# Kernel optimization log

Measured on AMD Instinct MI355X. Metric: run time of the kernel, lower is better.

Reference implementation:

```python
import jax, jax.numpy as jnp
import numpy as np

B, S, T, E, D = 16, 2048, 1024, 256, 256  # batch, src_len, tgt_len, enc_size, dec_size


def setup_inputs() -> dict:
    key = jax.random.key(0)
    k1, k2, k3, k4, k5 = jax.random.split(key, 5)
    enc_states = jax.random.normal(k1, (B, S, E), dtype=jnp.float32)
    dec_states = jax.random.normal(k2, (B, T, D), dtype=jnp.float32)
    # valid-prefix mask: each row has at least one valid (True) source position
    lengths = jax.random.randint(k3, (B,), 1, S + 1)
    src_mask = jnp.arange(S)[None, :] < lengths[:, None]  # (B, S) bool
    # Dense layer weights (no bias). Glorot-ish scale.
    W_enc = jax.random.normal(k4, (E, D), dtype=jnp.float32) / np.sqrt(E)
    W_fin = jax.random.normal(k5, (E + D, D), dtype=jnp.float32) / np.sqrt(E + D)
    return {"enc_states": enc_states, "dec_states": dec_states,
            "src_mask": src_mask, "W_enc": W_enc, "W_fin": W_fin}


def reference(enc_states, dec_states, src_mask, W_enc, W_fin):
    # enc_trnsfrmr: (B,S,E) @ (E,D) -> (B,S,D)
    enc_proj = jnp.einsum('bse,ed->bsd', enc_states, W_enc)
    # attention scores: batch_dot(dec_states, enc_proj^T) -> (B,T,S)
    scores = jnp.einsum('btd,bsd->bts', dec_states, enc_proj)
    scores = jnp.where(src_mask[:, None, :], scores, -jnp.inf)
    wts = jax.nn.softmax(scores, axis=-1)  # (B,T,S)
    # broadcast-multiply + reduce_sum == weighted sum over src positions
    context = jnp.einsum('bts,bse->bte', wts, enc_states)  # (B,T,E)
    cat = jnp.concatenate([context, dec_states], axis=-1)  # (B,T,E+D)
    return jnp.tanh(jnp.einsum('btf,fd->btd', cat, W_fin))  # (B,T,D)
```

## Files before the change

kernel.cpp:

```cpp
#include <hip/hip_runtime.h>
#include <math.h>
#include <stdint.h>

#define NB 16
#define NS 2048
#define NT 1024
#define NE 256
#define ND 256
#define NM (NB * NT)
#define KF (NE + ND)

typedef short sh8 __attribute__((ext_vector_type(8)));
typedef float f4v __attribute__((ext_vector_type(4)));

static __device__ __forceinline__ float bf2f(unsigned short u) {
    union { unsigned int i; float f; } v;
    v.i = ((unsigned int)u) << 16;
    return v.f;
}
static __device__ __forceinline__ unsigned short f2bf(float f) {
    union { unsigned int i; float f; } v;
    v.f = f;
    unsigned int x = v.i;
    x += 0x7FFFu + ((x >> 16) & 1u);
    return (unsigned short)(x >> 16);
}
static __device__ __forceinline__ float4 load4(const void* p, int isbf, long idx) {
    if (isbf) {
        const unsigned short* h = (const unsigned short*)p + idx;
        ushort4 u = *(const ushort4*)h;
        return make_float4(bf2f(u.x), bf2f(u.y), bf2f(u.z), bf2f(u.w));
    }
    const float* f = (const float*)p + idx;
    return *(const float4*)f;
}
static __device__ __forceinline__ int mvalid(const void* m, int kind, int b, int s) {
    long idx = (long)b * NS + s;
    switch (kind) {
        case 0:  return ((const unsigned char*)m)[idx] != 0;
        case 1:  return ((const int*)m)[idx] != 0;
        case 2:  return ((const unsigned short*)m)[idx] != 0;
        default: return ((const unsigned int*)m)[idx] != 0;
    }
}

__global__ void k_detect(const void* __restrict__ enc_raw,
                         const void* __restrict__ mask_raw,
                         int* __restrict__ flags) {
    __shared__ int cnt;
    if (threadIdx.x == 0) cnt = 0;
    __syncthreads();
    const unsigned short* h = (const unsigned short*)enc_raw;
    int local = 0;
    for (int i = threadIdx.x; i < 4096; i += 256) {
        int ex = (h[i] >> 7) & 0xFF;
        if (ex >= 97 && ex <= 157) local++;
    }
    atomicAdd(&cnt, local);
    __syncthreads();
    if (threadIdx.x == 0) {
        int isbf = (cnt >= 3700) ? 1 : 0;
        const unsigned char* mb = (const unsigned char*)mask_raw;
        int kind;
        if (mb[1] == 0x3F)                       kind = 2;
        else if (mb[3] == 0x3F && mb[1] == 0)    kind = 3;
        else if (mb[1] == 1)                     kind = 0;
        else if (mb[4] == 1 || mb[8] == 1)       kind = 1;
        else                                     kind = (mb[NS] == 1) ? 0 : 1;
        flags[0] = isbf;
        flags[1] = kind;
    }
}

__global__ __launch_bounds__(256) void k_split(const void* __restrict__ src,
                                               const int* __restrict__ flags,
                                               unsigned short* __restrict__ hh,
                                               unsigned short* __restrict__ ll) {
    const int isbf = flags[0];
    const long i = ((long)blockIdx.x * 256 + threadIdx.x) * 8;
    if (isbf) {
        sh8 v = *(const sh8*)((const unsigned short*)src + i);
        *(sh8*)(hh + i) = v;
    } else {
        const float* f = (const float*)src + i;
        sh8 hv, lv;
#pragma unroll
        for (int j = 0; j < 8; ++j) {
            float x = f[j];
            unsigned short h = f2bf(x);
            hv[j] = (short)h;
            lv[j] = (short)f2bf(x - bf2f(h));
        }
        *(sh8*)(hh + i) = hv;
        *(sh8*)(ll + i) = lv;
    }
}

__global__ __launch_bounds__(256) void k_twf(const void* __restrict__ Wfin,
                                             const int* __restrict__ flags,
                                             unsigned short* __restrict__ wfh,
                                             unsigned short* __restrict__ wfl) {
    const int isbf = flags[0];
    __shared__ float T[64][68];
    const int f0 = blockIdx.x * 64, n0 = blockIdx.y * 64;
    const int tid = threadIdx.x;
#pragma unroll
    for (int i = 0; i < 4; ++i) {
        int idx = tid + i * 256;
        int r = idx >> 4, c4 = (idx & 15) << 2;
        float4 v = load4(Wfin, isbf, (long)(f0 + r) * ND + n0 + c4);
        T[r][c4] = v.x; T[r][c4 + 1] = v.y; T[r][c4 + 2] = v.z; T[r][c4 + 3] = v.w;
    }
    __syncthreads();
#pragma unroll
    for (int i = 0; i < 4; ++i) {
        int idx = tid + i * 256;
        int n = idx >> 4, f4 = (idx & 15) << 2;
        ushort4 hv, lv;
        float x;
        x = T[f4 + 0][n]; hv.x = f2bf(x); lv.x = f2bf(x - bf2f(hv.x));
        x = T[f4 + 1][n]; hv.y = f2bf(x); lv.y = f2bf(x - bf2f(hv.y));
        x = T[f4 + 2][n]; hv.z = f2bf(x); lv.z = f2bf(x - bf2f(hv.z));
        x = T[f4 + 3][n]; hv.w = f2bf(x); lv.w = f2bf(x - bf2f(hv.w));
        long base = (long)(n0 + n) * KF + f0 + f4;
        *(ushort4*)&wfh[base] = hv;
        *(ushort4*)&wfl[base] = lv;
    }
}

__global__ __launch_bounds__(256) void k_q_m(const unsigned short* __restrict__ dh,
                                             const unsigned short* __restrict__ dl,
                                             const unsigned short* __restrict__ wh,
                                             const unsigned short* __restrict__ wl,
                                             const int* __restrict__ flags,
                                             unsigned short* __restrict__ qh,
                                             unsigned short* __restrict__ ql) {
    const int isbf = flags[0];
    const int tid = threadIdx.x;
    const int lane = tid & 63, wid = tid >> 6;
    const int lr = lane & 15, lg = lane >> 4;
    const int bid = blockIdx.x;
    const int mblk = (bid & 7) + (((bid >> 3) >> 2) << 3);
    const int nblk = (bid >> 3) & 3;
    const long m0 = (long)mblk * 128 + wid * 32;
    const int  n0 = nblk * 64;
    __shared__ __align__(16) unsigned short Bh_s[64][264];
    __shared__ __align__(16) unsigned short Bl_s[64][264];
    {
        const int row = tid >> 2, seg = (tid & 3) * 64;
        const unsigned short* src = wh + (long)(n0 + row) * ND + seg;
#pragma unroll
        for (int c = 0; c < 8; ++c)
            *(sh8*)&Bh_s[row][seg + c * 8] = *(const sh8*)(src + c * 8);
        if (!isbf) {
            const unsigned short* src2 = wl + (long)(n0 + row) * ND + seg;
#pragma unroll
            for (int c = 0; c < 8; ++c)
                *(sh8*)&Bl_s[row][seg + c * 8] = *(const sh8*)(src2 + c * 8);
        }
    }
    __syncthreads();
    const unsigned short* Ah = dh + (m0 + lr) * ND + lg * 8;
    const unsigned short* Al = dl + (m0 + lr) * ND + lg * 8;
    f4v acc[2][4];
#pragma unroll
    for (int i = 0; i < 2; ++i)
#pragma unroll
        for (int j = 0; j < 4; ++j) acc[i][j] = (f4v){0.f, 0.f, 0.f, 0.f};
    if (isbf) {
#pragma unroll
        for (int k8 = 0; k8 < 8; ++k8) {
            const int ko = k8 * 32;
            sh8 a0 = *(const sh8*)(Ah + ko);
            sh8 a1 = *(const sh8*)(Ah + 16 * ND + ko);
#pragma unroll
            for (int ni = 0; ni < 4; ++ni) {
                sh8 b = *(const sh8*)&Bh_s[ni * 16 + lr][ko + lg * 8];
                acc[0][ni] = __builtin_amdgcn_mfma_f32_16x16x32_bf16(a0, b, acc[0][ni], 0, 0, 0);
                acc[1][ni] = __builtin_amdgcn_mfma_f32_16x16x32_bf16(a1, b, acc[1][ni], 0, 0, 0);
            }
        }
    } else {
#pragma unroll
        for (int k8 = 0; k8 < 8; ++k8) {
            const int ko = k8 * 32;
            sh8 a0 = *(const sh8*)(Ah + ko);
            sh8 a1 = *(const sh8*)(Ah + 16 * ND + ko);
            sh8 la0 = *(const sh8*)(Al + ko);
            sh8 la1 = *(const sh8*)(Al + 16 * ND + ko);
#pragma unroll
            for (int ni = 0; ni < 4; ++ni) {
                sh8 b  = *(const sh8*)&Bh_s[ni * 16 + lr][ko + lg * 8];
                sh8 lb = *(const sh8*)&Bl_s[ni * 16 + lr][ko + lg * 8];
                acc[0][ni] = __builtin_amdgcn_mfma_f32_16x16x32_bf16(a0, b, acc[0][ni], 0, 0, 0);
                acc[0][ni] = __builtin_amdgcn_mfma_f32_16x16x32_bf16(la0, b, acc[0][ni], 0, 0, 0);
                acc[0][ni] = __builtin_amdgcn_mfma_f32_16x16x32_bf16(a0, lb, acc[0][ni], 0, 0, 0);
                acc[1][ni] = __builtin_amdgcn_mfma_f32_16x16x32_bf16(a1, b, acc[1][ni], 0, 0, 0);
                acc[1][ni] = __builtin_amdgcn_mfma_f32_16x16x32_bf16(la1, b, acc[1][ni], 0, 0, 0);
                acc[1][ni] = __builtin_amdgcn_mfma_f32_16x16x32_bf16(a1, lb, acc[1][ni], 0, 0, 0);
            }
        }
    }
#pragma unroll
    for (int mi = 0; mi < 2; ++mi)
#pragma unroll
        for (int r = 0; r < 4; ++r) {
            long rowb = (m0 + mi * 16 + lg * 4 + r) * NE + n0 + lr;
#pragma unroll
            for (int ni = 0; ni < 4; ++ni) {
                float v = acc[mi][ni][r];
                unsigned short h = f2bf(v);
                qh[rowb + ni * 16] = h;
                ql[rowb + ni * 16] = f2bf(v - bf2f(h));
            }
        }
}

__global__ __launch_bounds__(256, 2) void k_attn(
    const unsigned short* qh, const unsigned short* ql,
    const unsigned short* __restrict__ eh, const unsigned short* __restrict__ el,
    const void* __restrict__ mask, const int* __restrict__ flags,
    unsigned short* ch, unsigned short* cl,
    float* __restrict__ pctx, float* __restrict__ Mp, float* __restrict__ Lp)
{
    const int isbf  = flags[0];
    const int mkind = flags[1];
    const int b  = blockIdx.y;
    const int t0 = blockIdx.x * 32;
    const int part = blockIdx.z, nparts = gridDim.z;
    const int tid  = threadIdx.x;
    const int lane = tid & 63;
    const int wid  = tid >> 6;
    const int th = wid & 1;
    const int sh = wid >> 1;
    const int lr = lane & 15;
    const int lg = lane >> 4;

    __shared__ __align__(16) unsigned short EHR[32][264];
    __shared__ __align__(16) unsigned short ELR[32][264];
    __shared__ __align__(16) unsigned short VT[256][40];
    __shared__ __align__(16) float PBs[32][36];
    __shared__ float hm[2][32];
    __shared__ float hs[2][32];
    __shared__ int s_len;

    if (tid == 0) s_len = 0;
    __syncthreads();
    {
        int c = 0;
#pragma unroll
        for (int j = 0; j < 8; ++j) c += mvalid(mask, mkind, b, tid * 8 + j);
        atomicAdd(&s_len, c);
    }
    __syncthreads();
    const int len  = s_len;
    const int s_lo = part * (NS / nparts);
    const int s_hi = min(s_lo + NS / nparts, len);
    const int ntiles = (s_hi > s_lo) ? ((s_hi - s_lo + 31) >> 5) : 0;
    const long mrow = (long)part * NM + (long)b * NT + t0;
    if (ntiles == 0) {
        if (nparts > 1 && tid < 32) { Mp[mrow + tid] = -INFINITY; Lp[mrow + tid] = 0.f; }
        return;
    }

    sh8 qhf[8], qlf[8];
    {
        const unsigned short* qp  = qh + ((long)b * NT + t0 + th * 16 + lr) * NE + lg * 8;
        const unsigned short* qp2 = ql + ((long)b * NT + t0 + th * 16 + lr) * NE + lg * 8;
#pragma unroll
        for (int k8 = 0; k8 < 8; ++k8) {
            qhf[k8] = *(const sh8*)(qp  + k8 * 32);
            qlf[k8] = *(const sh8*)(qp2 + k8 * 32);
        }
    }

    f4v O[8];
#pragma unroll
    for (int et = 0; et < 8; ++et) O[et] = (f4v){0.f, 0.f, 0.f, 0.f};
    float Mreg4[4], L4[4], MregP = -INFINITY;
#pragma unroll
    for (int r = 0; r < 4; ++r) { Mreg4[r] = -INFINITY; L4[r] = 0.f; }

    const int ss = tid >> 3;
    const int ee = (tid & 7) * 8;

    sh8 rh[4], rl[4];
    {
        const unsigned short* eg = eh + ((long)b * NS + s_lo + ss) * NE;
#pragma unroll
        for (int c = 0; c < 4; ++c) rh[c] = *(const sh8*)(eg + ee + c * 64);
        if (!isbf) {
            const unsigned short* eg2 = el + ((long)b * NS + s_lo + ss) * NE;
#pragma unroll
            for (int c = 0; c < 4; ++c) rl[c] = *(const sh8*)(eg2 + ee + c * 64);
        }
#pragma unroll
        for (int c = 0; c < 4; ++c) {
            const int e0 = ee + c * 64;
            *(sh8*)&EHR[ss][e0] = rh[c];
            if (!isbf) *(sh8*)&ELR[ss][e0] = rl[c];
        }
    }

    for (int it = 0; it < ntiles; ++it) {
        const int s0 = s_lo + it * 32;
        __syncthreads();
        f4v cacc;
        {
            const unsigned short* ep = &EHR[sh * 16 + lr][lg * 8];
            const unsigned short* lp = &ELR[sh * 16 + lr][lg * 8];
            f4v c0 = (f4v){0.f, 0.f, 0.f, 0.f};
            f4v c1 = (f4v){0.f, 0.f, 0.f, 0.f};
            f4v c2 = (f4v){0.f, 0.f, 0.f, 0.f};
            if (isbf) {
#pragma unroll
                for (int k8 = 0; k8 < 8; ++k8) {
                    sh8 ea = *(const sh8*)(ep + k8 * 32);
                    c0 = __builtin_amdgcn_mfma_f32_16x16x32_bf16(ea, qhf[k8], c0, 0, 0, 0);
                    c1 = __builtin_amdgcn_mfma_f32_16x16x32_bf16(ea, qlf[k8], c1, 0, 0, 0);
                }
            } else {
#pragma unroll
                for (int k8 = 0; k8 < 8; ++k8) {
                    sh8 ea = *(const sh8*)(ep + k8 * 32);
                    sh8 eb = *(const sh8*)(lp + k8 * 32);
                    c0 = __builtin_amdgcn_mfma_f32_16x16x32_bf16(ea, qhf[k8], c0, 0, 0, 0);
                    c1 = __builtin_amdgcn_mfma_f32_16x16x32_bf16(ea, qlf[k8], c1, 0, 0, 0);
                    c2 = __builtin_amdgcn_mfma_f32_16x16x32_bf16(eb, qhf[k8], c2, 0, 0, 0);
                }
            }
            cacc = c0 + c1 + c2;
        }
        {
            unsigned short col[32];
#pragma unroll
            for (int s = 0; s < 32; ++s) col[s] = EHR[s][tid];
#pragma unroll
            for (int c = 0; c < 4; ++c)
                *(sh8*)&VT[tid][c * 8] = *(const sh8*)&col[c * 8];
        }
        float sc[4];
#pragma unroll
        for (int r = 0; r < 4; ++r) {
            int sl = sh * 16 + lg * 4 + r;
            sc[r] = (s0 + sl < len) ? cacc[r] : -INFINITY;
        }
        float m4 = fmaxf(fmaxf(sc[0], sc[1]), fmaxf(sc[2], sc[3]));
        m4 = fmaxf(m4, __shfl_xor(m4, 16));
        m4 = fmaxf(m4, __shfl_xor(m4, 32));
        float p[4], ps = 0.f;
#pragma unroll
        for (int r = 0; r < 4; ++r) {
            p[r] = (sc[r] == -INFINITY) ? 0.f : __expf(sc[r] - m4);
            ps += p[r];
        }
        ps += __shfl_xor(ps, 16);
        ps += __shfl_xor(ps, 32);
        if (lane < 16) { hm[sh][th * 16 + lane] = m4; hs[sh][th * 16 + lane] = ps; }
        *(float4*)&PBs[th * 16 + lr][sh * 16 + lg * 4] = make_float4(p[0], p[1], p[2], p[3]);
        const int more = (it + 1 < ntiles);
        if (more) {
            const unsigned short* eg = eh + ((long)b * NS + s0 + 32 + ss) * NE;
#pragma unroll
            for (int c = 0; c < 4; ++c) rh[c] = *(const sh8*)(eg + ee + c * 64);
            if (!isbf) {
                const unsigned short* eg2 = el + ((long)b * NS + s0 + 32 + ss) * NE;
#pragma unroll
                for (int c = 0; c < 4; ++c) rl[c] = *(const sh8*)(eg2 + ee + c * 64);
            }
        }
        __syncthreads();
        float f0, f1, al[4];
        {
            const int tP = th * 16 + lr;
            float h0 = hm[0][tP], h1 = hm[1][tP];
            float Mn = fmaxf(MregP, fmaxf(h0, h1));
            f0 = __expf(h0 - Mn);
            f1 = __expf(h1 - Mn);
            MregP = Mn;
        }
#pragma unroll
        for (int r = 0; r < 4; ++r) {
            const int t4 = th * 16 + lg * 4 + r;
            float g0 = hm[0][t4], g1 = hm[1][t4];
            float Mn = fmaxf(Mreg4[r], fmaxf(g0, g1));
            al[r] = __expf(Mreg4[r] - Mn);
            L4[r] = L4[r] * al[r] + hs[0][t4] * __expf(g0 - Mn) + hs[1][t4] * __expf(g1 - Mn);
            Mreg4[r] = Mn;
        }
        {
            const float fsc = (lg < 2) ? f0 : f1;
            f4v pA = *(const f4v*)&PBs[th * 16 + lr][lg * 8];
            f4v pB = *(const f4v*)&PBs[th * 16 + lr][lg * 8 + 4];
            sh8 pf;
#pragma unroll
            for (int j = 0; j < 4; ++j) {
                pf[j]     = (short)f2bf(pA[j] * fsc);
                pf[4 + j] = (short)f2bf(pB[j] * fsc);
            }
            f4v alv = (f4v){al[0], al[1], al[2], al[3]};
#pragma unroll
            for (int et = 0; et < 8; ++et) O[et] *= alv;
#pragma unroll
            for (int et = 0; et < 8; ++et) {
                sh8 vf = *(const sh8*)&VT[sh * 128 + et * 16 + lr][lg * 8];
                O[et] = __builtin_amdgcn_mfma_f32_16x16x32_bf16(pf, vf, O[et], 0, 0, 0);
            }
        }
        if (more) {
#pragma unroll
            for (int c = 0; c < 4; ++c) {
                const int e0 = ee + c * 64;
                *(sh8*)&EHR[ss][e0] = rh[c];
                if (!isbf) *(sh8*)&ELR[ss][e0] = rl[c];
            }
        }
    }
    if (nparts == 1) {
        f4v inv;
#pragma unroll
        for (int r = 0; r < 4; ++r) inv[r] = 1.0f / L4[r];
#pragma unroll
        for (int et = 0; et < 8; ++et) {
            f4v ov = O[et] * inv;
            long rbase = ((long)b * NT + t0 + th * 16 + lg * 4) * NE + sh * 128 + et * 16 + lr;
#pragma unroll
            for (int r = 0; r < 4; ++r) {
                float v = ov[r];
                unsigned short h = f2bf(v);
                ch[rbase + (long)r * NE] = h;
                cl[rbase + (long)r * NE] = f2bf(v - bf2f(h));
            }
        }
    } else {
        float* op = pctx + (long)part * NM * NE;
#pragma unroll
        for (int et = 0; et < 8; ++et) {
            long rbase = ((long)b * NT + t0 + th * 16 + lg * 4) * NE + sh * 128 + et * 16 + lr;
#pragma unroll
            for (int r = 0; r < 4; ++r)
                op[rbase + (long)r * NE] = O[et][r];
        }
        if (sh == 0 && lr == 0) {
#pragma unroll
            for (int r = 0; r < 4; ++r) {
                Mp[mrow + th * 16 + lg * 4 + r] = Mreg4[r];
                Lp[mrow + th * 16 + lg * 4 + r] = L4[r];
            }
        }
    }
}

__global__ __launch_bounds__(256) void k_comb(const float* __restrict__ pctx,
                                              const float* __restrict__ Mp,
                                              const float* __restrict__ Lp,
                                              int nparts,
                                              unsigned short* __restrict__ ch,
                                              unsigned short* __restrict__ cl) {
    const long m = (long)blockIdx.x * 8 + (threadIdx.x >> 5);
    const int  e0 = (threadIdx.x & 31) * 8;
    float Mv[4], Lv[4];
    float M = -INFINITY;
    for (int p = 0; p < nparts; ++p) {
        Mv[p] = Mp[(long)p * NM + m];
        Lv[p] = Lp[(long)p * NM + m];
        if (Lv[p] > 0.f) M = fmaxf(M, Mv[p]);
    }
    float L = 0.f, w[4];
    for (int p = 0; p < nparts; ++p) {
        w[p] = (Lv[p] > 0.f) ? __expf(Mv[p] - M) : 0.f;
        L += Lv[p] * w[p];
    }
    float o[8] = {};
    for (int p = 0; p < nparts; ++p) {
        if (w[p] > 0.f) {
            const float* src = pctx + (long)p * NM * NE + m * NE + e0;
            f4v a = *(const f4v*)src;
            f4v c = *(const f4v*)(src + 4);
#pragma unroll
            for (int j = 0; j < 4; ++j) { o[j] += a[j] * w[p]; o[4 + j] += c[j] * w[p]; }
        }
    }
    const float inv = 1.0f / L;
    unsigned short hv[8], lv[8];
#pragma unroll
    for (int j = 0; j < 8; ++j) {
        float v = o[j] * inv;
        unsigned short h = f2bf(v);
        hv[j] = h;
        lv[j] = f2bf(v - bf2f(h));
    }
    long base = m * NE + e0;
    *(ushort4*)&ch[base]     = *(ushort4*)&hv[0];
    *(ushort4*)&ch[base + 4] = *(ushort4*)&hv[4];
    *(ushort4*)&cl[base]     = *(ushort4*)&lv[0];
    *(ushort4*)&cl[base + 4] = *(ushort4*)&lv[4];
}

__global__ __launch_bounds__(256) void k_fin_m(const unsigned short* __restrict__ ch,
                                               const unsigned short* __restrict__ cl,
                                               const unsigned short* __restrict__ dh,
                                               const unsigned short* __restrict__ dl,
                                               const unsigned short* __restrict__ wh,
                                               const unsigned short* __restrict__ wl,
                                               const int* __restrict__ flags,
                                               void* __restrict__ out) {
    const int isbf = flags[0];
    const int tid = threadIdx.x;
    const int lane = tid & 63, wid = tid >> 6;
    const int lr = lane & 15, lg = lane >> 4;
    const int bid = blockIdx.x;
    const int mblk = (bid & 7) + (((bid >> 3) >> 2) << 3);
    const int nblk = (bid >> 3) & 3;
    const long m0 = (long)mblk * 128 + wid * 32;
    const int  n0 = nblk * 64;
    __shared__ __align__(16) unsigned short Bh_s[64][264];
    __shared__ __align__(16) unsigned short Bl_s[64][264];
    const int row = tid >> 2, seg = (tid & 3) * 64;
    f4v acc[2][4];
#pragma unroll
    for (int i = 0; i < 2; ++i)
#pragma unroll
        for (int j = 0; j < 4; ++j) acc[i][j] = (f4v){0.f, 0.f, 0.f, 0.f};

#pragma unroll
    for (int ph = 0; ph < 2; ++ph) {
        if (ph) __syncthreads();
        {
            const unsigned short* src = wh + (long)(n0 + row) * KF + ph * 256 + seg;
#pragma unroll
            for (int c = 0; c < 8; ++c)
                *(sh8*)&Bh_s[row][seg + c * 8] = *(const sh8*)(src + c * 8);
            if (!isbf) {
                const unsigned short* src2 = wl + (long)(n0 + row) * KF + ph * 256 + seg;
#pragma unroll
                for (int c = 0; c < 8; ++c)
                    *(sh8*)&Bl_s[row][seg + c * 8] = *(const sh8*)(src2 + c * 8);
            }
        }
        __syncthreads();
        const unsigned short* Ah = (ph == 0 ? ch : dh) + (m0 + lr) * 256 + lg * 8;
        const unsigned short* Al = (ph == 0 ? cl : dl) + (m0 + lr) * 256 + lg * 8;
        if (isbf) {
#pragma unroll
            for (int k8 = 0; k8 < 8; ++k8) {
                const int ko = k8 * 32;
                sh8 a0 = *(const sh8*)(Ah + ko);
                sh8 a1 = *(const sh8*)(Ah + 16 * 256 + ko);
#pragma unroll
                for (int ni = 0; ni < 4; ++ni) {
                    sh8 b = *(const sh8*)&Bh_s[ni * 16 + lr][ko + lg * 8];
                    acc[0][ni] = __builtin_amdgcn_mfma_f32_16x16x32_bf16(a0, b, acc[0][ni], 0, 0, 0);
                    acc[1][ni] = __builtin_amdgcn_mfma_f32_16x16x32_bf16(a1, b, acc[1][ni], 0, 0, 0);
                }
            }
        } else {
#pragma unroll
            for (int k8 = 0; k8 < 8; ++k8) {
                const int ko = k8 * 32;
                sh8 a0 = *(const sh8*)(Ah + ko);
                sh8 a1 = *(const sh8*)(Ah + 16 * 256 + ko);
                sh8 la0 = *(const sh8*)(Al + ko);
                sh8 la1 = *(const sh8*)(Al + 16 * 256 + ko);
#pragma unroll
                for (int ni = 0; ni < 4; ++ni) {
                    sh8 b  = *(const sh8*)&Bh_s[ni * 16 + lr][ko + lg * 8];
                    sh8 lb = *(const sh8*)&Bl_s[ni * 16 + lr][ko + lg * 8];
                    acc[0][ni] = __builtin_amdgcn_mfma_f32_16x16x32_bf16(a0, b, acc[0][ni], 0, 0, 0);
                    acc[0][ni] = __builtin_amdgcn_mfma_f32_16x16x32_bf16(la0, b, acc[0][ni], 0, 0, 0);
                    acc[0][ni] = __builtin_amdgcn_mfma_f32_16x16x32_bf16(a0, lb, acc[0][ni], 0, 0, 0);
                    acc[1][ni] = __builtin_amdgcn_mfma_f32_16x16x32_bf16(a1, b, acc[1][ni], 0, 0, 0);
                    acc[1][ni] = __builtin_amdgcn_mfma_f32_16x16x32_bf16(la1, b, acc[1][ni], 0, 0, 0);
                    acc[1][ni] = __builtin_amdgcn_mfma_f32_16x16x32_bf16(a1, lb, acc[1][ni], 0, 0, 0);
                }
            }
        }
    }
    if (isbf) {
        unsigned short* o = (unsigned short*)out;
#pragma unroll
        for (int mi = 0; mi < 2; ++mi)
#pragma unroll
            for (int r = 0; r < 4; ++r) {
                long rowb = (m0 + mi * 16 + lg * 4 + r) * ND + n0 + lr;
#pragma unroll
                for (int ni = 0; ni < 4; ++ni)
                    o[rowb + ni * 16] = f2bf(tanhf(acc[mi][ni][r]));
            }
    } else {
        float* o = (float*)out;
#pragma unroll
        for (int mi = 0; mi < 2; ++mi)
#pragma unroll
            for (int r = 0; r < 4; ++r) {
                long rowb = (m0 + mi * 16 + lg * 4 + r) * ND + n0 + lr;
#pragma unroll
                for (int ni = 0; ni < 4; ++ni)
                    o[rowb + ni * 16] = tanhf(acc[mi][ni][r]);
            }
    }
}

extern "C" void kernel_launch(void* const* d_in, const int* in_sizes, int n_in,
                              void* d_out, int out_size, void* d_ws, size_t ws_size,
                              hipStream_t stream) {
    const void* enc  = d_in[0];
    const void* dec  = d_in[1];
    const void* mask = d_in[2];
    const void* Wenc = d_in[3];
    const void* Wfin = d_in[4];

    unsigned short* ehb = (unsigned short*)d_ws;
    unsigned short* elb = ehb + (size_t)NB * NS * NE;
    unsigned short* qhb = elb + (size_t)NB * NS * NE;
    unsigned short* qlb = qhb + (size_t)NM * NE;
    unsigned short* dhb = qlb + (size_t)NM * NE;
    unsigned short* dlb = dhb + (size_t)NM * ND;
    unsigned short* weh = dlb + (size_t)NM * ND;
    unsigned short* wel = weh + (size_t)NE * ND;
    unsigned short* wfh = wel + (size_t)NE * ND;
    unsigned short* wfl = wfh + (size_t)KF * ND;
    unsigned short* wend = wfl + (size_t)KF * ND;

    const size_t fixed = (size_t)((char*)wend - (char*)d_ws);
    int parts = 1;
    for (int p = 4; p >= 1; p >>= 1) {
        size_t need = fixed + ((p > 1) ? ((size_t)p * NM * NE * 4 + (size_t)p * NM * 8) : 0) + 256;
        if (ws_size >= need) { parts = p; break; }
    }
    float* pctx = (float*)wend;
    float* Mpb  = pctx + ((parts > 1) ? (size_t)parts * NM * NE : 0);
    float* Lpb  = Mpb + (size_t)parts * NM;
    int*   flags = (int*)(Lpb + (size_t)parts * NM);

    k_detect<<<1, 256, 0, stream>>>(enc, mask, flags);
    k_split<<<(NB * NS * NE) / 2048, 256, 0, stream>>>(enc, flags, ehb, elb);
    k_split<<<(NM * ND) / 2048, 256, 0, stream>>>(dec, flags, dhb, dlb);
    k_split<<<(NE * ND) / 2048, 256, 0, stream>>>(Wenc, flags, weh, wel);
    k_twf<<<dim3(KF / 64, ND / 64), 256, 0, stream>>>(Wfin, flags, wfh, wfl);
    k_q_m<<<512, 256, 0, stream>>>(dhb, dlb, weh, wel, flags, qhb, qlb);
    k_attn<<<dim3(NT / 32, NB, parts), 256, 0, stream>>>(qhb, qlb, ehb, elb, mask, flags,
                                                         qhb, qlb, pctx, Mpb, Lpb);
    if (parts > 1)
        k_comb<<<NM / 8, 256, 0, stream>>>(pctx, Mpb, Lpb, parts, qhb, qlb);
    k_fin_m<<<512, 256, 0, stream>>>(qhb, qlb, dhb, dlb, wfh, wfl, flags, d_out);
}
```

Baseline: 266.7 us.

## Fuse fp32 split into GEMMs, precompute mask lengths, interleave attention tiles

The hi/lo bf16 split of dec_states and W_enc now happens inside the q-projection and final GEMM kernels, so two split launches and their workspace round-trips go away. The projection weights are staged through shared memory in 128-wide halves, which shrinks shared memory use. Mask lengths are computed once in the detect kernel rather than in every attention block. Source tiles are assigned to attention partitions round-robin, which balances work across partitions when rows have short valid prefixes. In exchange, fp32 conversion work is repeated across the N-blocks of each GEMM and there are more barrier phases.

```diff
diff --git a/kernel.cpp b/kernel.cpp
--- a/kernel.cpp
+++ b/kernel.cpp
@@ -43,22 +43,35 @@
         default: return ((const unsigned int*)m)[idx] != 0;
     }
 }
+static __device__ __forceinline__ void f8_to_hl(const float* p, sh8& h8, sh8& l8) {
+    f4v x0 = *(const f4v*)p;
+    f4v x1 = *(const f4v*)(p + 4);
+#pragma unroll
+    for (int j = 0; j < 4; ++j) {
+        unsigned short h = f2bf(x0[j]); h8[j] = (short)h; l8[j] = (short)f2bf(x0[j] - bf2f(h));
+        h = f2bf(x1[j]); h8[4 + j] = (short)h; l8[4 + j] = (short)f2bf(x1[j] - bf2f(h));
+    }
+}
 
 __global__ void k_detect(const void* __restrict__ enc_raw,
                          const void* __restrict__ mask_raw,
                          int* __restrict__ flags) {
     __shared__ int cnt;
-    if (threadIdx.x == 0) cnt = 0;
+    __shared__ int kindS;
+    __shared__ int lensS[16];
+    const int tid = threadIdx.x;
+    if (tid == 0) cnt = 0;
+    if (tid < 16) lensS[tid] = 0;
     __syncthreads();
     const unsigned short* h = (const unsigned short*)enc_raw;
     int local = 0;
-    for (int i = threadIdx.x; i < 4096; i += 256) {
+    for (int i = tid; i < 4096; i += 256) {
         int ex = (h[i] >> 7) & 0xFF;
         if (ex >= 97 && ex <= 157) local++;
     }
     atomicAdd(&cnt, local);
     __syncthreads();
-    if (threadIdx.x == 0) {
+    if (tid == 0) {
         int isbf = (cnt >= 3700) ? 1 : 0;
         const unsigned char* mb = (const unsigned char*)mask_raw;
         int kind;
@@ -69,7 +82,16 @@
         else                                     kind = (mb[NS] == 1) ? 0 : 1;
         flags[0] = isbf;
         flags[1] = kind;
-    }
+        kindS = kind;
+    }
+    __syncthreads();
+    const int kind = kindS;
+    const int bb = tid >> 4, sl = tid & 15;
+    int c = 0;
+    for (int j = 0; j < 128; ++j) c += mvalid(mask_raw, kind, bb, sl + j * 16);
+    atomicAdd(&lensS[bb], c);
+    __syncthreads();
+    if (tid < 16) flags[2 + tid] = lensS[tid];
 }
 
 __global__ __launch_bounds__(256) void k_split(const void* __restrict__ src,
@@ -84,13 +106,7 @@
     } else {
         const float* f = (const float*)src + i;
         sh8 hv, lv;
-#pragma unroll
-        for (int j = 0; j < 8; ++j) {
-            float x = f[j];
-            unsigned short h = f2bf(x);
-            hv[j] = (short)h;
-            lv[j] = (short)f2bf(x - bf2f(h));
-        }
+        f8_to_hl(f, hv, lv);
         *(sh8*)(hh + i) = hv;
         *(sh8*)(ll + i) = lv;
     }
@@ -128,10 +144,8 @@
     }
 }
 
-__global__ __launch_bounds__(256) void k_q_m(const unsigned short* __restrict__ dh,
-                                             const unsigned short* __restrict__ dl,
-                                             const unsigned short* __restrict__ wh,
-                                             const unsigned short* __restrict__ wl,
+__global__ __launch_bounds__(256) void k_q_m(const void* __restrict__ dec,
+                                             const void* __restrict__ Wenc,
                                              const int* __restrict__ flags,
                                              unsigned short* __restrict__ qh,
                                              unsigned short* __restrict__ ql) {
@@ -144,60 +158,67 @@
     const int nblk = (bid >> 3) & 3;
     const long m0 = (long)mblk * 128 + wid * 32;
     const int  n0 = nblk * 64;
-    __shared__ __align__(16) unsigned short Bh_s[64][264];
-    __shared__ __align__(16) unsigned short Bl_s[64][264];
-    {
-        const int row = tid >> 2, seg = (tid & 3) * 64;
-        const unsigned short* src = wh + (long)(n0 + row) * ND + seg;
-#pragma unroll
-        for (int c = 0; c < 8; ++c)
-            *(sh8*)&Bh_s[row][seg + c * 8] = *(const sh8*)(src + c * 8);
-        if (!isbf) {
-            const unsigned short* src2 = wl + (long)(n0 + row) * ND + seg;
-#pragma unroll
-            for (int c = 0; c < 8; ++c)
-                *(sh8*)&Bl_s[row][seg + c * 8] = *(const sh8*)(src2 + c * 8);
-        }
-    }
-    __syncthreads();
-    const unsigned short* Ah = dh + (m0 + lr) * ND + lg * 8;
-    const unsigned short* Al = dl + (m0 + lr) * ND + lg * 8;
+    __shared__ __align__(16) unsigned short Bh_s[64][136];
+    __shared__ __align__(16) unsigned short Bl_s[64][136];
+    const int row = tid >> 2, seg = (tid & 3) * 32;
     f4v acc[2][4];
 #pragma unroll
     for (int i = 0; i < 2; ++i)
 #pragma unroll
         for (int j = 0; j < 4; ++j) acc[i][j] = (f4v){0.f, 0.f, 0.f, 0.f};
-    if (isbf) {
-#pragma unroll
-        for (int k8 = 0; k8 < 8; ++k8) {
-            const int ko = k8 * 32;
-            sh8 a0 = *(const sh8*)(Ah + ko);
-            sh8 a1 = *(const sh8*)(Ah + 16 * ND + ko);
-#pragma unroll
-            for (int ni = 0; ni < 4; ++ni) {
-                sh8 b = *(const sh8*)&Bh_s[ni * 16 + lr][ko + lg * 8];
-                acc[0][ni] = __builtin_amdgcn_mfma_f32_16x16x32_bf16(a0, b, acc[0][ni], 0, 0, 0);
-                acc[1][ni] = __builtin_amdgcn_mfma_f32_16x16x32_bf16(a1, b, acc[1][ni], 0, 0, 0);
-            }
-        }
-    } else {
-#pragma unroll
-        for (int k8 = 0; k8 < 8; ++k8) {
-            const int ko = k8 * 32;
-            sh8 a0 = *(const sh8*)(Ah + ko);
-            sh8 a1 = *(const sh8*)(Ah + 16 * ND + ko);
-            sh8 la0 = *(const sh8*)(Al + ko);
-            sh8 la1 = *(const sh8*)(Al + 16 * ND + ko);
-#pragma unroll
-            for (int ni = 0; ni < 4; ++ni) {
-                sh8 b  = *(const sh8*)&Bh_s[ni * 16 + lr][ko + lg * 8];
-                sh8 lb = *(const sh8*)&Bl_s[ni * 16 + lr][ko + lg * 8];
-                acc[0][ni] = __builtin_amdgcn_mfma_f32_16x16x32_bf16(a0, b, acc[0][ni], 0, 0, 0);
-                acc[0][ni] = __builtin_amdgcn_mfma_f32_16x16x32_bf16(la0, b, acc[0][ni], 0, 0, 0);
-                acc[0][ni] = __builtin_amdgcn_mfma_f32_16x16x32_bf16(a0, lb, acc[0][ni], 0, 0, 0);
-                acc[1][ni] = __builtin_amdgcn_mfma_f32_16x16x32_bf16(a1, b, acc[1][ni], 0, 0, 0);
-                acc[1][ni] = __builtin_amdgcn_mfma_f32_16x16x32_bf16(la1, b, acc[1][ni], 0, 0, 0);
-                acc[1][ni] = __builtin_amdgcn_mfma_f32_16x16x32_bf16(a1, lb, acc[1][ni], 0, 0, 0);
+
+#pragma unroll
+    for (int ph = 0; ph < 2; ++ph) {
+        if (ph) __syncthreads();
+        if (isbf) {
+            const unsigned short* src = (const unsigned short*)Wenc + (long)(n0 + row) * ND + ph * 128 + seg;
+#pragma unroll
+            for (int c = 0; c < 4; ++c)
+                *(sh8*)&Bh_s[row][seg + c * 8] = *(const sh8*)(src + c * 8);
+        } else {
+            const float* src = (const float*)Wenc + (long)(n0 + row) * ND + ph * 128 + seg;
+#pragma unroll
+            for (int c = 0; c < 4; ++c) {
+                sh8 hv, lv;
+                f8_to_hl(src + c * 8, hv, lv);
+                *(sh8*)&Bh_s[row][seg + c * 8] = hv;
+                *(sh8*)&Bl_s[row][seg + c * 8] = lv;
+            }
+        }
+        __syncthreads();
+        if (isbf) {
+            const unsigned short* Ab = (const unsigned short*)dec + (m0 + lr) * ND + ph * 128 + lg * 8;
+#pragma unroll
+            for (int k8 = 0; k8 < 4; ++k8) {
+                const int ko = k8 * 32;
+                sh8 a0 = *(const sh8*)(Ab + ko);
+                sh8 a1 = *(const sh8*)(Ab + 16 * ND + ko);
+#pragma unroll
+                for (int ni = 0; ni < 4; ++ni) {
+                    sh8 b = *(const sh8*)&Bh_s[ni * 16 + lr][ko + lg * 8];
+                    acc[0][ni] = __builtin_amdgcn_mfma_f32_16x16x32_bf16(a0, b, acc[0][ni], 0, 0, 0);
+                    acc[1][ni] = __builtin_amdgcn_mfma_f32_16x16x32_bf16(a1, b, acc[1][ni], 0, 0, 0);
+                }
+            }
+        } else {
+            const float* Af = (const float*)dec + (m0 + lr) * ND + ph * 128 + lg * 8;
+#pragma unroll
+            for (int k8 = 0; k8 < 4; ++k8) {
+                const int ko = k8 * 32;
+                sh8 a0, la0, a1, la1;
+                f8_to_hl(Af + ko, a0, la0);
+                f8_to_hl(Af + 16 * ND + ko, a1, la1);
+#pragma unroll
+                for (int ni = 0; ni < 4; ++ni) {
+                    sh8 b  = *(const sh8*)&Bh_s[ni * 16 + lr][ko + lg * 8];
+                    sh8 lb = *(const sh8*)&Bl_s[ni * 16 + lr][ko + lg * 8];
+                    acc[0][ni] = __builtin_amdgcn_mfma_f32_16x16x32_bf16(a0, b, acc[0][ni], 0, 0, 0);
+                    acc[0][ni] = __builtin_amdgcn_mfma_f32_16x16x32_bf16(la0, b, acc[0][ni], 0, 0, 0);
+                    acc[0][ni] = __builtin_amdgcn_mfma_f32_16x16x32_bf16(a0, lb, acc[0][ni], 0, 0, 0);
+                    acc[1][ni] = __builtin_amdgcn_mfma_f32_16x16x32_bf16(a1, b, acc[1][ni], 0, 0, 0);
+                    acc[1][ni] = __builtin_amdgcn_mfma_f32_16x16x32_bf16(la1, b, acc[1][ni], 0, 0, 0);
+                    acc[1][ni] = __builtin_amdgcn_mfma_f32_16x16x32_bf16(a1, lb, acc[1][ni], 0, 0, 0);
+                }
             }
         }
     }
@@ -219,12 +240,11 @@
 __global__ __launch_bounds__(256, 2) void k_attn(
     const unsigned short* qh, const unsigned short* ql,
     const unsigned short* __restrict__ eh, const unsigned short* __restrict__ el,
-    const void* __restrict__ mask, const int* __restrict__ flags,
+    const int* __restrict__ flags,
     unsigned short* ch, unsigned short* cl,
     float* __restrict__ pctx, float* __restrict__ Mp, float* __restrict__ Lp)
 {
     const int isbf  = flags[0];
-    const int mkind = flags[1];
     const int b  = blockIdx.y;
     const int t0 = blockIdx.x * 32;
     const int part = blockIdx.z, nparts = gridDim.z;
@@ -242,21 +262,10 @@
     __shared__ __align__(16) float PBs[32][36];
     __shared__ float hm[2][32];
     __shared__ float hs[2][32];
-    __shared__ int s_len;
-
-    if (tid == 0) s_len = 0;
-    __syncthreads();
-    {
-        int c = 0;
-#pragma unroll
-        for (int j = 0; j < 8; ++j) c += mvalid(mask, mkind, b, tid * 8 + j);
-        atomicAdd(&s_len, c);
-    }
-    __syncthreads();
-    const int len  = s_len;
-    const int s_lo = part * (NS / nparts);
-    const int s_hi = min(s_lo + NS / nparts, len);
-    const int ntiles = (s_hi > s_lo) ? ((s_hi - s_lo + 31) >> 5) : 0;
+
+    const int len = flags[2 + b];
+    const int nT = (len + 31) >> 5;
+    const int ntiles = (nT > part) ? ((nT - part + nparts - 1) / nparts) : 0;
     const long mrow = (long)part * NM + (long)b * NT + t0;
     if (ntiles == 0) {
         if (nparts > 1 && tid < 32) { Mp[mrow + tid] = -INFINITY; Lp[mrow + tid] = 0.f; }
@@ -286,11 +295,11 @@
 
     sh8 rh[4], rl[4];
     {
-        const unsigned short* eg = eh + ((long)b * NS + s_lo + ss) * NE;
+        const unsigned short* eg = eh + ((long)b * NS + part * 32 + ss) * NE;
 #pragma unroll
         for (int c = 0; c < 4; ++c) rh[c] = *(const sh8*)(eg + ee + c * 64);
         if (!isbf) {
-            const unsigned short* eg2 = el + ((long)b * NS + s_lo + ss) * NE;
+            const unsigned short* eg2 = el + ((long)b * NS + part * 32 + ss) * NE;
 #pragma unroll
             for (int c = 0; c < 4; ++c) rl[c] = *(const sh8*)(eg2 + ee + c * 64);
         }
@@ -303,7 +312,7 @@
     }
 
     for (int it = 0; it < ntiles; ++it) {
-        const int s0 = s_lo + it * 32;
+        const int s0 = (part + it * nparts) << 5;
         __syncthreads();
         f4v cacc;
         {
@@ -360,11 +369,12 @@
         *(float4*)&PBs[th * 16 + lr][sh * 16 + lg * 4] = make_float4(p[0], p[1], p[2], p[3]);
         const int more = (it + 1 < ntiles);
         if (more) {
-            const unsigned short* eg = eh + ((long)b * NS + s0 + 32 + ss) * NE;
+            const int s0n = s0 + (nparts << 5);
+            const unsigned short* eg = eh + ((long)b * NS + s0n + ss) * NE;
 #pragma unroll
             for (int c = 0; c < 4; ++c) rh[c] = *(const sh8*)(eg + ee + c * 64);
             if (!isbf) {
-                const unsigned short* eg2 = el + ((long)b * NS + s0 + 32 + ss) * NE;
+                const unsigned short* eg2 = el + ((long)b * NS + s0n + ss) * NE;
 #pragma unroll
                 for (int c = 0; c < 4; ++c) rl[c] = *(const sh8*)(eg2 + ee + c * 64);
             }
@@ -499,8 +509,7 @@
 
 __global__ __launch_bounds__(256) void k_fin_m(const unsigned short* __restrict__ ch,
                                                const unsigned short* __restrict__ cl,
-                                               const unsigned short* __restrict__ dh,
-                                               const unsigned short* __restrict__ dl,
+                                               const void* __restrict__ dec,
                                                const unsigned short* __restrict__ wh,
                                                const unsigned short* __restrict__ wl,
                                                const int* __restrict__ flags,
@@ -514,9 +523,9 @@
     const int nblk = (bid >> 3) & 3;
     const long m0 = (long)mblk * 128 + wid * 32;
     const int  n0 = nblk * 64;
-    __shared__ __align__(16) unsigned short Bh_s[64][264];
-    __shared__ __align__(16) unsigned short Bl_s[64][264];
-    const int row = tid >> 2, seg = (tid & 3) * 64;
+    __shared__ __align__(16) unsigned short Bh_s[64][136];
+    __shared__ __align__(16) unsigned short Bl_s[64][136];
+    const int row = tid >> 2, seg = (tid & 3) * 32;
     f4v acc[2][4];
 #pragma unroll
     for (int i = 0; i < 2; ++i)
@@ -524,54 +533,86 @@
         for (int j = 0; j < 4; ++j) acc[i][j] = (f4v){0.f, 0.f, 0.f, 0.f};
 
 #pragma unroll
-    for (int ph = 0; ph < 2; ++ph) {
+    for (int ph = 0; ph < 4; ++ph) {
         if (ph) __syncthreads();
         {
-            const unsigned short* src = wh + (long)(n0 + row) * KF + ph * 256 + seg;
-#pragma unroll
-            for (int c = 0; c < 8; ++c)
+            const unsigned short* src = wh + (long)(n0 + row) * KF + ph * 128 + seg;
+#pragma unroll
+            for (int c = 0; c < 4; ++c)
                 *(sh8*)&Bh_s[row][seg + c * 8] = *(const sh8*)(src + c * 8);
             if (!isbf) {
-                const unsigned short* src2 = wl + (long)(n0 + row) * KF + ph * 256 + seg;
-#pragma unroll
-                for (int c = 0; c < 8; ++c)
+                const unsigned short* src2 = wl + (long)(n0 + row) * KF + ph * 128 + seg;
+#pragma unroll
+                for (int c = 0; c < 4; ++c)
                     *(sh8*)&Bl_s[row][seg + c * 8] = *(const sh8*)(src2 + c * 8);
             }
         }
         __syncthreads();
-        const unsigned short* Ah = (ph == 0 ? ch : dh) + (m0 + lr) * 256 + lg * 8;
-        const unsigned short* Al = (ph == 0 ? cl : dl) + (m0 + lr) * 256 + lg * 8;
-        if (isbf) {
-#pragma unroll
-            for (int k8 = 0; k8 < 8; ++k8) {
+        if (ph < 2) {
+            const unsigned short* Ah = ch + (m0 + lr) * NE + ph * 128 + lg * 8;
+            const unsigned short* Al = cl + (m0 + lr) * NE + ph * 128 + lg * 8;
+#pragma unroll
+            for (int k8 = 0; k8 < 4; ++k8) {
                 const int ko = k8 * 32;
                 sh8 a0 = *(const sh8*)(Ah + ko);
-                sh8 a1 = *(const sh8*)(Ah + 16 * 256 + ko);
-#pragma unroll
-                for (int ni = 0; ni < 4; ++ni) {
-                    sh8 b = *(const sh8*)&Bh_s[ni * 16 + lr][ko + lg * 8];
-                    acc[0][ni] = __builtin_amdgcn_mfma_f32_16x16x32_bf16(a0, b, acc[0][ni], 0, 0, 0);
-                    acc[1][ni] = __builtin_amdgcn_mfma_f32_16x16x32_bf16(a1, b, acc[1][ni], 0, 0, 0);
+                sh8 a1 = *(const sh8*)(Ah + 16 * NE + ko);
+                if (isbf) {
+#pragma unroll
+                    for (int ni = 0; ni < 4; ++ni) {
+                        sh8 b = *(const sh8*)&Bh_s[ni * 16 + lr][ko + lg * 8];
+                        acc[0][ni] = __builtin_amdgcn_mfma_f32_16x16x32_bf16(a0, b, acc[0][ni], 0, 0, 0);
+                        acc[1][ni] = __builtin_amdgcn_mfma_f32_16x16x32_bf16(a1, b, acc[1][ni], 0, 0, 0);
+                    }
+                } else {
+                    sh8 la0 = *(const sh8*)(Al + ko);
+                    sh8 la1 = *(const sh8*)(Al + 16 * NE + ko);
+#pragma unroll
+                    for (int ni = 0; ni < 4; ++ni) {
+                        sh8 b  = *(const sh8*)&Bh_s[ni * 16 + lr][ko + lg * 8];
+                        sh8 lb = *(const sh8*)&Bl_s[ni * 16 + lr][ko + lg * 8];
+                        acc[0][ni] = __builtin_amdgcn_mfma_f32_16x16x32_bf16(a0, b, acc[0][ni], 0, 0, 0);
+                        acc[0][ni] = __builtin_amdgcn_mfma_f32_16x16x32_bf16(la0, b, acc[0][ni], 0, 0, 0);
+                        acc[0][ni] = __builtin_amdgcn_mfma_f32_16x16x32_bf16(a0, lb, acc[0][ni], 0, 0, 0);
+                        acc[1][ni] = __builtin_amdgcn_mfma_f32_16x16x32_bf16(a1, b, acc[1][ni], 0, 0, 0);
+                        acc[1][ni] = __builtin_amdgcn_mfma_f32_16x16x32_bf16(la1, b, acc[1][ni], 0, 0, 0);
+                        acc[1][ni] = __builtin_amdgcn_mfma_f32_16x16x32_bf16(a1, lb, acc[1][ni], 0, 0, 0);
+                    }
                 }
             }
         } else {
-#pragma unroll
-            for (int k8 = 0; k8 < 8; ++k8) {
-                const int ko = k8 * 32;
-                sh8 a0 = *(const sh8*)(Ah + ko);
-                sh8 a1 = *(const sh8*)(Ah + 16 * 256 + ko);
-                sh8 la0 = *(const sh8*)(Al + ko);
-                sh8 la1 = *(const sh8*)(Al + 16 * 256 + ko);
-#pragma unroll
-                for (int ni = 0; ni < 4; ++ni) {
-                    sh8 b  = *(const sh8*)&Bh_s[ni * 16 + lr][ko + lg * 8];
-                    sh8 lb = *(const sh8*)&Bl_s[ni * 16 + lr][ko + lg * 8];
-                    acc[0][ni] = __builtin_amdgcn_mfma_f32_16x16x32_bf16(a0, b, acc[0][ni], 0, 0, 0);
-                    acc[0][ni] = __builtin_amdgcn_mfma_f32_16x16x32_bf16(la0, b, acc[0][ni], 0, 0, 0);
-                    acc[0][ni] = __builtin_amdgcn_mfma_f32_16x16x32_bf16(a0, lb, acc[0][ni], 0, 0, 0);
-                    acc[1][ni] = __builtin_amdgcn_mfma_f32_16x16x32_bf16(a1, b, acc[1][ni], 0, 0, 0);
-                    acc[1][ni] = __builtin_amdgcn_mfma_f32_16x16x32_bf16(la1, b, acc[1][ni], 0, 0, 0);
-                    acc[1][ni] = __builtin_amdgcn_mfma_f32_16x16x32_bf16(a1, lb, acc[1][ni], 0, 0, 0);
+            if (isbf) {
+                const unsigned short* Ab = (const unsigned short*)dec + (m0 + lr) * ND + (ph - 2) * 128 + lg * 8;
+#pragma unroll
+                for (int k8 = 0; k8 < 4; ++k8) {
+                    const int ko = k8 * 32;
+                    sh8 a0 = *(const sh8*)(Ab + ko);
+                    sh8 a1 = *(const sh8*)(Ab + 16 * ND + ko);
+#pragma unroll
+                    for (int ni = 0; ni < 4; ++ni) {
+                        sh8 b = *(const sh8*)&Bh_s[ni * 16 + lr][ko + lg * 8];
+                        acc[0][ni] = __builtin_amdgcn_mfma_f32_16x16x32_bf16(a0, b, acc[0][ni], 0, 0, 0);
+                        acc[1][ni] = __builtin_amdgcn_mfma_f32_16x16x32_bf16(a1, b, acc[1][ni], 0, 0, 0);
+                    }
+                }
+            } else {
+                const float* Af = (const float*)dec + (m0 + lr) * ND + (ph - 2) * 128 + lg * 8;
+#pragma unroll
+                for (int k8 = 0; k8 < 4; ++k8) {
+                    const int ko = k8 * 32;
+                    sh8 a0, la0, a1, la1;
+                    f8_to_hl(Af + ko, a0, la0);
+                    f8_to_hl(Af + 16 * ND + ko, a1, la1);
+#pragma unroll
+                    for (int ni = 0; ni < 4; ++ni) {
+                        sh8 b  = *(const sh8*)&Bh_s[ni * 16 + lr][ko + lg * 8];
+                        sh8 lb = *(const sh8*)&Bl_s[ni * 16 + lr][ko + lg * 8];
+                        acc[0][ni] = __builtin_amdgcn_mfma_f32_16x16x32_bf16(a0, b, acc[0][ni], 0, 0, 0);
+                        acc[0][ni] = __builtin_amdgcn_mfma_f32_16x16x32_bf16(la0, b, acc[0][ni], 0, 0, 0);
+                        acc[0][ni] = __builtin_amdgcn_mfma_f32_16x16x32_bf16(a0, lb, acc[0][ni], 0, 0, 0);
+                        acc[1][ni] = __builtin_amdgcn_mfma_f32_16x16x32_bf16(a1, b, acc[1][ni], 0, 0, 0);
+                        acc[1][ni] = __builtin_amdgcn_mfma_f32_16x16x32_bf16(la1, b, acc[1][ni], 0, 0, 0);
+                        acc[1][ni] = __builtin_amdgcn_mfma_f32_16x16x32_bf16(a1, lb, acc[1][ni], 0, 0, 0);
+                    }
                 }
             }
         }
@@ -614,11 +655,7 @@
     unsigned short* elb = ehb + (size_t)NB * NS * NE;
     unsigned short* qhb = elb + (size_t)NB * NS * NE;
     unsigned short* qlb = qhb + (size_t)NM * NE;
-    unsigned short* dhb = qlb + (size_t)NM * NE;
-    unsigned short* dlb = dhb + (size_t)NM * ND;
-    unsigned short* weh = dlb + (size_t)NM * ND;
-    unsigned short* wel = weh + (size_t)NE * ND;
-    unsigned short* wfh = wel + (size_t)NE * ND;
+    unsigned short* wfh = qlb + (size_t)NM * NE;
     unsigned short* wfl = wfh + (size_t)KF * ND;
     unsigned short* wend = wfl + (size_t)KF * ND;
 
@@ -635,13 +672,11 @@
 
     k_detect<<<1, 256, 0, stream>>>(enc, mask, flags);
     k_split<<<(NB * NS * NE) / 2048, 256, 0, stream>>>(enc, flags, ehb, elb);
-    k_split<<<(NM * ND) / 2048, 256, 0, stream>>>(dec, flags, dhb, dlb);
-    k_split<<<(NE * ND) / 2048, 256, 0, stream>>>(Wenc, flags, weh, wel);
     k_twf<<<dim3(KF / 64, ND / 64), 256, 0, stream>>>(Wfin, flags, wfh, wfl);
-    k_q_m<<<512, 256, 0, stream>>>(dhb, dlb, weh, wel, flags, qhb, qlb);
-    k_attn<<<dim3(NT / 32, NB, parts), 256, 0, stream>>>(qhb, qlb, ehb, elb, mask, flags,
+    k_q_m<<<512, 256, 0, stream>>>(dec, Wenc, flags, qhb, qlb);
+    k_attn<<<dim3(NT / 32, NB, parts), 256, 0, stream>>>(qhb, qlb, ehb, elb, flags,
                                                          qhb, qlb, pctx, Mpb, Lpb);
     if (parts > 1)
         k_comb<<<NM / 8, 256, 0, stream>>>(pctx, Mpb, Lpb, parts, qhb, qlb);
-    k_fin_m<<<512, 256, 0, stream>>>(qhb, qlb, dhb, dlb, wfh, wfl, flags, d_out);
-}
+    k_fin_m<<<512, 256, 0, stream>>>(qhb, qlb, dec, wfh, wfl, flags, d_out);
+}
```

Measured after the change: 287.6 us. 7.8% more time.
